# Performance work log

Hardware: AMD Instinct MI355X
Metric: run time of the kernel (lower is better)

Reference implementation:

```python
import jax, jax.numpy as jnp
import numpy as np

N, E, IN, H = 20000, 50000, 32, 64


def _lin_init(k, fan_in, shape):
    b = 1.0 / np.sqrt(fan_in)
    return jax.random.uniform(k, shape, jnp.float32, -b, b)


def setup_inputs() -> dict:
    key = jax.random.key(0)
    ks = jax.random.split(key, 16)
    inp = {
        "x": jax.random.normal(ks[0], (N, IN), jnp.float32),
        "edge_index": jax.random.randint(ks[1], (2, E), 0, N, dtype=jnp.int32),
        "edge_attr": jax.random.normal(ks[2], (E, 1, 2), jnp.float32),
        # layer 0: edge MLP 2->H->IN*H, root [IN,H], bias [H]
        "w1_0": _lin_init(ks[3], 2, (2, H)),
        "b1_0": _lin_init(ks[4], 2, (H,)),
        "w2_0": _lin_init(ks[5], H, (H, IN * H)),
        "b2_0": _lin_init(ks[6], H, (IN * H,)),
        "root_0": _lin_init(ks[7], IN, (IN, H)),
        "bias_0": _lin_init(ks[8], IN, (H,)),
        # layer 1: edge MLP 2->H->H*H, root [H,H], bias [H]
        "w1_1": _lin_init(ks[9], 2, (2, H)),
        "b1_1": _lin_init(ks[10], 2, (H,)),
        "w2_1": _lin_init(ks[11], H, (H, H * H)),
        "b2_1": _lin_init(ks[12], H, (H * H,)),
        "root_1": _lin_init(ks[13], H, (H, H)),
        "bias_1": _lin_init(ks[14], H, (H,)),
    }
    return inp


def _nnconv(x, src, dst, ea, w1, b1, w2, b2, root, bias, in_c, out_c):
    # per-edge weight matrices from edge-attr MLP: [E, in_c*out_c]
    h = jax.nn.relu(ea @ w1 + b1) @ w2 + b2
    W = h.reshape(-1, in_c, out_c)                     # [E, in, out]
    msg = jnp.einsum('ei,eio->eo', x[src], W)          # gather + per-edge matmul
    agg = jax.ops.segment_sum(msg, dst, num_segments=x.shape[0])  # scatter-add
    return agg + x @ root + bias                       # add aggr (PyG NNConv, aggr='add')


def reference(x, edge_index, edge_attr,
              w1_0, b1_0, w2_0, b2_0, root_0, bias_0,
              w1_1, b1_1, w2_1, b2_1, root_1, bias_1):
    src, dst = edge_index[0], edge_index[1]
    ea = edge_attr.reshape(edge_attr.shape[0], 2)      # [E, 2]
    x = jax.nn.relu(_nnconv(x, src, dst, ea, w1_0, b1_0, w2_0, b2_0, root_0, bias_0, IN, H))
    x = jax.nn.relu(_nnconv(x, src, dst, ea, w1_1, b1_1, w2_1, b2_1, root_1, bias_1, H, H))
    return x
```

## Files before the change

### kernel.cpp

```cpp
#include <hip/hip_runtime.h>

typedef _Float16 v8h __attribute__((ext_vector_type(8)));
typedef float v16f __attribute__((ext_vector_type(16)));

__global__ void prep_fused(const float* __restrict__ w2_0, const float* __restrict__ b2_0,
                           _Float16* __restrict__ BF0,
                           const float* __restrict__ w2_1, const float* __restrict__ b2_1,
                           _Float16* __restrict__ BF1,
                           const float* __restrict__ x, const float* __restrict__ root,
                           const float* __restrict__ bias, float* __restrict__ agg,
                           _Float16* __restrict__ xb, int N) {
    int idx = blockIdx.x * 256 + threadIdx.x;
    const int n0 = 264 * 512;
    const int n1 = 528 * 512;
    if (idx < n0 + n1) {
        const float* w2; const float* b2; _Float16* BF; int IN, rel;
        if (idx < n0) { w2 = w2_0; b2 = b2_0; BF = BF0; IN = 32; rel = idx; }
        else          { w2 = w2_1; b2 = b2_1; BF = BF1; IN = 64; rel = idx - n0; }
        int j = rel & 7, lane = (rel >> 3) & 63, f = rel >> 9;
        int nf = f & 1, kk16 = f >> 1;
        int ln = lane & 31, g2 = lane >> 5;
        int k = kk16 * 16 + g2 * 8 + j;
        int ko = k / IN, i = k - ko * IN;
        int o = nf * 32 + ln;
        float v = (ko < 64) ? w2[ko * (IN * 64) + i * 64 + o]
                : (ko == 64 ? b2[i * 64 + o] : 0.f);
        BF[rel] = (_Float16)v;
        return;
    }
    idx -= (n0 + n1);
    if (idx >= N * 64) return;
    int n = idx >> 6, o = idx & 63;
    float s = bias[o];
    const float* xr = x + (size_t)n * 32;
    #pragma unroll 8
    for (int i = 0; i < 32; ++i) s += xr[i] * root[i * 64 + o];
    agg[idx] = s;
    if (o < 32) xb[n * 32 + o] = (_Float16)xr[o];
}

__global__ void mid_kernel(const float* __restrict__ agg0, const float* __restrict__ root1,
                           const float* __restrict__ bias1, _Float16* __restrict__ x1b,
                           float* __restrict__ agg1, int N) {
    int idx = blockIdx.x * 256 + threadIdx.x;
    if (idx >= N * 64) return;
    int n = idx >> 6, o = idx & 63;
    const float* ar = agg0 + (size_t)n * 64;
    float s = bias1[o];
    #pragma unroll 8
    for (int i = 0; i < 64; ++i) s += fmaxf(ar[i], 0.f) * root1[i * 64 + o];
    agg1[idx] = s;
    x1b[idx] = (_Float16)fmaxf(agg0[idx], 0.f);
}

__global__ void final_relu(const float* __restrict__ agg1, float* __restrict__ out, int n) {
    int idx = blockIdx.x * 256 + threadIdx.x;
    if (idx < n) out[idx] = fmaxf(agg1[idx], 0.f);
}

template<int IN_C>
__global__ __launch_bounds__(512, 1)
void edge_gemm(const float* __restrict__ ea,
               const float* __restrict__ w1, const float* __restrict__ b1,
               const _Float16* __restrict__ xb, const _Float16* __restrict__ BF,
               const int* __restrict__ srcI, const int* __restrict__ dstI,
               float* __restrict__ agg, int E) {
    constexpr int PH  = IN_C / 16;
    constexpr int CPR = IN_C / 8;
    constexpr int M   = 256;

    constexpr size_t XBYTES = (size_t)M * IN_C * 2;
    constexpr size_t RBYTES = (size_t)M * 66 * 2;
    constexpr size_t BBYTES = (size_t)M * 65 * 4;
    constexpr size_t SBYTES = (XBYTES + RBYTES > BBYTES) ? (XBYTES + RBYTES) : BBYTES;

    __shared__ __align__(16) char smem[SBYTES];
    __shared__ int sh_dst[M];
    auto sh_x  = (_Float16 (*)[IN_C])smem;
    auto sh_r1 = (_Float16 (*)[66])(smem + XBYTES);
    auto buf   = (float (*)[65])smem;

    int tid = threadIdx.x;
    int ebase = blockIdx.x * M;
    int valid = E - ebase; if (valid > M) valid = M;

    if (tid < M) {
        sh_dst[tid] = (tid < valid) ? dstI[ebase + tid] : 0;
        sh_r1[tid][64] = (_Float16)1.f;
        sh_r1[tid][65] = (_Float16)0.f;
    }
    for (int i = tid; i < M * 64; i += 512) {
        int e = i >> 6, j = i & 63;
        int ge = (e < valid) ? (ebase + e) : ebase;
        float2 av = *(const float2*)(ea + (size_t)ge * 2);
        sh_r1[e][j] = (_Float16)fmaxf(av.x * w1[j] + av.y * w1[64 + j] + b1[j], 0.f);
    }
    for (int i = tid; i < M * CPR; i += 512) {
        int r = i / CPR, c = i - r * CPR;
        int sidx = (r < valid) ? srcI[ebase + r] : 0;
        *(uint4*)&sh_x[r][c * 8] = *(const uint4*)(xb + (size_t)sidx * IN_C + (size_t)c * 8);
    }
    __syncthreads();

    int wv = tid >> 6, lane = tid & 63, ln = lane & 31, g2 = lane >> 5;
    int nf = wv & 1, kh = (wv >> 1) & 1, mh = wv >> 2;
    int mbase = mh * 128;

    v8h xs0[PH], xs1[PH], xs2[PH], xs3[PH];
    #pragma unroll
    for (int p = 0; p < PH; ++p) {
        xs0[p] = *(const v8h*)&sh_x[mbase + ln     ][p * 16 + g2 * 8];
        xs1[p] = *(const v8h*)&sh_x[mbase + ln + 32][p * 16 + g2 * 8];
        xs2[p] = *(const v8h*)&sh_x[mbase + ln + 64][p * 16 + g2 * 8];
        xs3[p] = *(const v8h*)&sh_x[mbase + ln + 96][p * 16 + g2 * 8];
    }

    v16f acc0 = {0,0,0,0,0,0,0,0,0,0,0,0,0,0,0,0};
    v16f acc1 = acc0, acc2 = acc0, acc3 = acc0;

    const uint4* bp = (const uint4*)BF + (size_t)nf * 64 + lane;
    int kb = kh * 33;

    uint4 b[PH], bn[PH];
    auto LD = [&](uint4 (&d)[PH], int ko) {
        #pragma unroll
        for (int p = 0; p < PH; ++p) d[p] = bp[(size_t)(ko * PH + p) * 128];
    };
    auto FM = [&](uint4 (&d)[PH], int ko) {
        _Float16 sv0 = sh_r1[mbase + ln     ][ko];
        _Float16 sv1 = sh_r1[mbase + ln + 32][ko];
        _Float16 sv2 = sh_r1[mbase + ln + 64][ko];
        _Float16 sv3 = sh_r1[mbase + ln + 96][ko];
        #pragma unroll
        for (int p = 0; p < PH; ++p) {
            v8h bb; __builtin_memcpy(&bb, &d[p], 16);
            acc0 = __builtin_amdgcn_mfma_f32_32x32x16_f16(xs0[p] * sv0, bb, acc0, 0, 0, 0);
            acc1 = __builtin_amdgcn_mfma_f32_32x32x16_f16(xs1[p] * sv1, bb, acc1, 0, 0, 0);
            acc2 = __builtin_amdgcn_mfma_f32_32x32x16_f16(xs2[p] * sv2, bb, acc2, 0, 0, 0);
            acc3 = __builtin_amdgcn_mfma_f32_32x32x16_f16(xs3[p] * sv3, bb, acc3, 0, 0, 0);
        }
    };

    LD(b, kb);
    #pragma unroll 1
    for (int t = 0; t < 16; ++t) {
        LD(bn, kb + 2 * t + 1);
        FM(b,  kb + 2 * t);
        LD(b,  kb + 2 * t + 2);
        FM(bn, kb + 2 * t + 1);
    }
    FM(b, kb + 32);

    int colb = nf * 32 + ln;
    __syncthreads();
    if (kh == 1) {
        #pragma unroll
        for (int r = 0; r < 16; ++r) {
            int row = mbase + 4 * g2 + (r & 3) + 8 * (r >> 2);
            buf[row     ][colb] = acc0[r];
            buf[row + 32][colb] = acc1[r];
            buf[row + 64][colb] = acc2[r];
            buf[row + 96][colb] = acc3[r];
        }
    }
    __syncthreads();
    if (kh == 0) {
        #pragma unroll
        for (int r = 0; r < 16; ++r) {
            int row = mbase + 4 * g2 + (r & 3) + 8 * (r >> 2);
            if (row < valid)
                atomicAdd(&agg[(size_t)sh_dst[row] * 64 + colb], acc0[r] + buf[row][colb]);
            int row1 = row + 32;
            if (row1 < valid)
                atomicAdd(&agg[(size_t)sh_dst[row1] * 64 + colb], acc1[r] + buf[row1][colb]);
            int row2 = row + 64;
            if (row2 < valid)
                atomicAdd(&agg[(size_t)sh_dst[row2] * 64 + colb], acc2[r] + buf[row2][colb]);
            int row3 = row + 96;
            if (row3 < valid)
                atomicAdd(&agg[(size_t)sh_dst[row3] * 64 + colb], acc3[r] + buf[row3][colb]);
        }
    }
}

extern "C" void kernel_launch(void* const* d_in, const int* in_sizes, int n_in,
                              void* d_out, int out_size, void* d_ws, size_t ws_size,
                              hipStream_t stream) {
    const float* x      = (const float*)d_in[0];
    const int*   ei     = (const int*)d_in[1];
    const float* ea     = (const float*)d_in[2];
    const float* w1_0   = (const float*)d_in[3];
    const float* b1_0   = (const float*)d_in[4];
    const float* w2_0   = (const float*)d_in[5];
    const float* b2_0   = (const float*)d_in[6];
    const float* root_0 = (const float*)d_in[7];
    const float* bias_0 = (const float*)d_in[8];
    const float* w1_1   = (const float*)d_in[9];
    const float* b1_1   = (const float*)d_in[10];
    const float* w2_1   = (const float*)d_in[11];
    const float* b2_1   = (const float*)d_in[12];
    const float* root_1 = (const float*)d_in[13];
    const float* bias_1 = (const float*)d_in[14];
    float* out = (float*)d_out;

    int N = in_sizes[0] / 32;
    int E = in_sizes[1] / 2;
    const int* srcI = ei;
    const int* dstI = ei + E;

    char* ws = (char*)d_ws;
    size_t off = 0;
    auto carve = [&](size_t bytes) {
        void* p = ws + off;
        off += (bytes + 255) & ~(size_t)255;
        return p;
    };
    _Float16* BF0  = (_Float16*)carve((size_t)264 * 512 * 2);
    _Float16* BF1  = (_Float16*)carve((size_t)528 * 512 * 2);
    _Float16* XB0  = (_Float16*)carve((size_t)N * 32 * 2);
    _Float16* X1B  = (_Float16*)carve((size_t)N * 64 * 2);
    float*    AGG0 = (float*)carve((size_t)N * 64 * 4);
    float*    AGG1 = (float*)carve((size_t)N * 64 * 4);

    int tprep = (264 + 528) * 512 + N * 64;
    prep_fused<<<(tprep + 255) / 256, 256, 0, stream>>>(w2_0, b2_0, BF0, w2_1, b2_1, BF1,
                                                        x, root_0, bias_0, AGG0, XB0, N);

    int gblocks = (E + 255) / 256;
    edge_gemm<32><<<gblocks, 512, 0, stream>>>(ea, w1_0, b1_0, XB0, BF0, srcI, dstI, AGG0, E);

    mid_kernel<<<(N * 64 + 255) / 256, 256, 0, stream>>>(AGG0, root_1, bias_1, X1B, AGG1, N);

    edge_gemm<64><<<gblocks, 512, 0, stream>>>(ea, w1_1, b1_1, X1B, BF1, srcI, dstI, AGG1, E);

    final_relu<<<(N * 64 + 255) / 256, 256, 0, stream>>>(AGG1, out, N * 64);
}
```

Measured before the change: 192.9 us.

## Drop K-split in edge GEMM; give each wave two M-subtiles over full K

```diff
diff --git a/kernel.cpp b/kernel.cpp
--- a/kernel.cpp
+++ b/kernel.cpp
@@ -68,17 +68,11 @@
     constexpr int PH  = IN_C / 16;
     constexpr int CPR = IN_C / 8;
     constexpr int M   = 256;
-
-    constexpr size_t XBYTES = (size_t)M * IN_C * 2;
-    constexpr size_t RBYTES = (size_t)M * 66 * 2;
-    constexpr size_t BBYTES = (size_t)M * 65 * 4;
-    constexpr size_t SBYTES = (XBYTES + RBYTES > BBYTES) ? (XBYTES + RBYTES) : BBYTES;
-
-    __shared__ __align__(16) char smem[SBYTES];
+    constexpr int NCH = M * CPR;
+
+    __shared__ __align__(16) uint4 sh_xf[NCH];
+    __shared__ _Float16 sh_r1[M][66];
     __shared__ int sh_dst[M];
-    auto sh_x  = (_Float16 (*)[IN_C])smem;
-    auto sh_r1 = (_Float16 (*)[66])(smem + XBYTES);
-    auto buf   = (float (*)[65])smem;
 
     int tid = threadIdx.x;
     int ebase = blockIdx.x * M;
@@ -87,7 +81,6 @@
     if (tid < M) {
         sh_dst[tid] = (tid < valid) ? dstI[ebase + tid] : 0;
         sh_r1[tid][64] = (_Float16)1.f;
-        sh_r1[tid][65] = (_Float16)0.f;
     }
     for (int i = tid; i < M * 64; i += 512) {
         int e = i >> 6, j = i & 63;
@@ -95,31 +88,32 @@
         float2 av = *(const float2*)(ea + (size_t)ge * 2);
         sh_r1[e][j] = (_Float16)fmaxf(av.x * w1[j] + av.y * w1[64 + j] + b1[j], 0.f);
     }
-    for (int i = tid; i < M * CPR; i += 512) {
-        int r = i / CPR, c = i - r * CPR;
+    for (int d = tid; d < NCH; d += 512) {
+        int ln = d & 31, g2 = (d >> 5) & 1;
+        int sp = d >> 6;
+        int p = sp & (PH - 1), s = sp / PH;
+        int r = s * 32 + ln;
+        int c = p * 2 + g2;
         int sidx = (r < valid) ? srcI[ebase + r] : 0;
-        *(uint4*)&sh_x[r][c * 8] = *(const uint4*)(xb + (size_t)sidx * IN_C + (size_t)c * 8);
+        sh_xf[d] = *(const uint4*)(xb + (size_t)sidx * IN_C + (size_t)c * 8);
     }
     __syncthreads();
 
     int wv = tid >> 6, lane = tid & 63, ln = lane & 31, g2 = lane >> 5;
-    int nf = wv & 1, kh = (wv >> 1) & 1, mh = wv >> 2;
-    int mbase = mh * 128;
-
-    v8h xs0[PH], xs1[PH], xs2[PH], xs3[PH];
+    int nf = wv & 1, q = wv >> 1;
+    int sg0 = q * 2, sg1 = q * 2 + 1;
+
+    v8h xs0[PH], xs1[PH];
     #pragma unroll
     for (int p = 0; p < PH; ++p) {
-        xs0[p] = *(const v8h*)&sh_x[mbase + ln     ][p * 16 + g2 * 8];
-        xs1[p] = *(const v8h*)&sh_x[mbase + ln + 32][p * 16 + g2 * 8];
-        xs2[p] = *(const v8h*)&sh_x[mbase + ln + 64][p * 16 + g2 * 8];
-        xs3[p] = *(const v8h*)&sh_x[mbase + ln + 96][p * 16 + g2 * 8];
+        xs0[p] = *(const v8h*)&sh_xf[((sg0 * PH + p) * 2 + g2) * 32 + ln];
+        xs1[p] = *(const v8h*)&sh_xf[((sg1 * PH + p) * 2 + g2) * 32 + ln];
     }
 
     v16f acc0 = {0,0,0,0,0,0,0,0,0,0,0,0,0,0,0,0};
-    v16f acc1 = acc0, acc2 = acc0, acc3 = acc0;
+    v16f acc1 = acc0;
 
     const uint4* bp = (const uint4*)BF + (size_t)nf * 64 + lane;
-    int kb = kh * 33;
 
     uint4 b[PH], bn[PH];
     auto LD = [&](uint4 (&d)[PH], int ko) {
@@ -127,59 +121,35 @@
         for (int p = 0; p < PH; ++p) d[p] = bp[(size_t)(ko * PH + p) * 128];
     };
     auto FM = [&](uint4 (&d)[PH], int ko) {
-        _Float16 sv0 = sh_r1[mbase + ln     ][ko];
-        _Float16 sv1 = sh_r1[mbase + ln + 32][ko];
-        _Float16 sv2 = sh_r1[mbase + ln + 64][ko];
-        _Float16 sv3 = sh_r1[mbase + ln + 96][ko];
+        _Float16 sv0 = sh_r1[sg0 * 32 + ln][ko];
+        _Float16 sv1 = sh_r1[sg1 * 32 + ln][ko];
         #pragma unroll
         for (int p = 0; p < PH; ++p) {
             v8h bb; __builtin_memcpy(&bb, &d[p], 16);
             acc0 = __builtin_amdgcn_mfma_f32_32x32x16_f16(xs0[p] * sv0, bb, acc0, 0, 0, 0);
             acc1 = __builtin_amdgcn_mfma_f32_32x32x16_f16(xs1[p] * sv1, bb, acc1, 0, 0, 0);
-            acc2 = __builtin_amdgcn_mfma_f32_32x32x16_f16(xs2[p] * sv2, bb, acc2, 0, 0, 0);
-            acc3 = __builtin_amdgcn_mfma_f32_32x32x16_f16(xs3[p] * sv3, bb, acc3, 0, 0, 0);
         }
     };
 
-    LD(b, kb);
+    LD(b, 0);
     #pragma unroll 1
-    for (int t = 0; t < 16; ++t) {
-        LD(bn, kb + 2 * t + 1);
-        FM(b,  kb + 2 * t);
-        LD(b,  kb + 2 * t + 2);
-        FM(bn, kb + 2 * t + 1);
-    }
-    FM(b, kb + 32);
+    for (int t = 0; t < 32; ++t) {
+        LD(bn, 2 * t + 1);
+        FM(b,  2 * t);
+        LD(b,  2 * t + 2);
+        FM(bn, 2 * t + 1);
+    }
+    FM(b, 64);
 
     int colb = nf * 32 + ln;
-    __syncthreads();
-    if (kh == 1) {
-        #pragma unroll
-        for (int r = 0; r < 16; ++r) {
-            int row = mbase + 4 * g2 + (r & 3) + 8 * (r >> 2);
-            buf[row     ][colb] = acc0[r];
-            buf[row + 32][colb] = acc1[r];
-            buf[row + 64][colb] = acc2[r];
-            buf[row + 96][colb] = acc3[r];
-        }
-    }
-    __syncthreads();
-    if (kh == 0) {
-        #pragma unroll
-        for (int r = 0; r < 16; ++r) {
-            int row = mbase + 4 * g2 + (r & 3) + 8 * (r >> 2);
-            if (row < valid)
-                atomicAdd(&agg[(size_t)sh_dst[row] * 64 + colb], acc0[r] + buf[row][colb]);
-            int row1 = row + 32;
-            if (row1 < valid)
-                atomicAdd(&agg[(size_t)sh_dst[row1] * 64 + colb], acc1[r] + buf[row1][colb]);
-            int row2 = row + 64;
-            if (row2 < valid)
-                atomicAdd(&agg[(size_t)sh_dst[row2] * 64 + colb], acc2[r] + buf[row2][colb]);
-            int row3 = row + 96;
-            if (row3 < valid)
-                atomicAdd(&agg[(size_t)sh_dst[row3] * 64 + colb], acc3[r] + buf[row3][colb]);
-        }
+    #pragma unroll
+    for (int r = 0; r < 16; ++r) {
+        int row = q * 64 + 4 * g2 + (r & 3) + 8 * (r >> 2);
+        if (row < valid)
+            atomicAdd(&agg[(size_t)sh_dst[row] * 64 + colb], acc0[r]);
+        int row1 = row + 32;
+        if (row1 < valid)
+            atomicAdd(&agg[(size_t)sh_dst[row1] * 64 + colb], acc1[r]);
     }
 }
 
```

After: 190.9 us. Within noise of the previous version (-1.1%).
